# Kernel tuning notes

Measured on AMD Instinct MI355X. Metric: run time of the kernel, lower is better.

The kernel has to match this reference:

```python
import jax, jax.numpy as jnp
import numpy as np

N = 100000
E = 1600000
IN_DIM, H1, H2, H3 = 128, 128, 64, 32


def gcn_conv(x, edge_index, W, b, n):
    # PyG GCNConv (default): add self-loops, symmetric norm D^-1/2 (A+I) D^-1/2,
    # out[dst] = sum_{src->dst} norm * (x @ W)[src] + b
    src, dst = edge_index[0], edge_index[1]
    loops = jnp.arange(n)
    src = jnp.concatenate([src, loops])
    dst = jnp.concatenate([dst, loops])
    deg = jax.ops.segment_sum(jnp.ones((src.shape[0],), dtype=x.dtype), dst, num_segments=n)
    dinv = jnp.where(deg > 0, jax.lax.rsqrt(deg), jnp.zeros((), dtype=x.dtype))
    norm = dinv[src] * dinv[dst]  # [E+N]
    h = x @ W                      # [N, out_dim] dense transform first (out_dim <= in_dim)
    msg = h[src] * norm[:, None]   # [E+N, out_dim] gather + scale
    out = jax.ops.segment_sum(msg, dst, num_segments=n)
    return out + b


def setup_inputs() -> dict:
    key = jax.random.key(0)
    ks = jax.random.split(key, 10)
    def glorot(k, shape):
        lim = np.sqrt(6.0 / (shape[0] + shape[1]))
        return jax.random.uniform(k, shape, jnp.float32, -lim, lim)
    return {
        "x": jax.random.normal(ks[0], (N, IN_DIM), jnp.float32),
        "edge_index": jax.random.randint(ks[1], (2, E), 0, N, jnp.int64),
        "W1": glorot(ks[2], (IN_DIM, H1)), "b1": jnp.zeros((H1,), jnp.float32),
        "W2": glorot(ks[3], (H1, H2)),     "b2": jnp.zeros((H2,), jnp.float32),
        "W3": glorot(ks[4], (H2, H3)),     "b3": jnp.zeros((H3,), jnp.float32),
        "Wl": glorot(ks[5], (H3, 1)),      "bl": jnp.zeros((1,), jnp.float32),
    }


def reference(x, edge_index, W1, b1, W2, b2, W3, b3, Wl, bl):
    n = x.shape[0]
    h = jax.nn.relu(gcn_conv(x, edge_index, W1, b1, n))   # dropout p=0.5 is identity in eval
    h = jax.nn.relu(gcn_conv(h, edge_index, W2, b2, n))
    h = jax.nn.relu(gcn_conv(h, edge_index, W3, b3, n))
    return jax.nn.sigmoid(h @ Wl + bl)                    # [N, 1]
```

## Files before the change

kernel.cpp:

```cpp
#include <hip/hip_runtime.h>
#include <hip/hip_fp16.h>
#include <math.h>


#define BSHIFT 8
#define BNODES (1 << BSHIFT)
#define SRCBITS 17
#define MAXB 512

union H8 { float4 f4; __half2 h2[4]; };

typedef _Float16 half8 __attribute__((ext_vector_type(8)));
typedef float floatx4 __attribute__((ext_vector_type(4)));


__global__ __launch_bounds__(256) void k_hist(const int* __restrict__ dst, int E,
                                              int* __restrict__ bucketcnt, int B) {
    __shared__ int h[MAXB];
    int tid = threadIdx.x;
    h[tid] = 0; h[tid + 256] = 0;
    __syncthreads();
    for (int i = blockIdx.x * 256 + tid; i < E; i += gridDim.x * 256)
        atomicAdd(&h[dst[i] >> BSHIFT], 1);
    __syncthreads();
    if (tid < B && h[tid] > 0) atomicAdd(&bucketcnt[tid], h[tid]);
    int t2 = tid + 256;
    if (t2 < B && h[t2] > 0) atomicAdd(&bucketcnt[t2], h[t2]);
}

__global__ __launch_bounds__(512) void k_bscan(const int* __restrict__ bucketcnt,
                                               int* __restrict__ bucketbase,
                                               int* __restrict__ bucketfill,
                                               int* __restrict__ row_ptr,
                                               int B, int n, int E) {
    __shared__ int s[MAXB];
    int tid = threadIdx.x;
    int v = (tid < B) ? bucketcnt[tid] : 0;
    s[tid] = v;
    __syncthreads();
    for (int off = 1; off < MAXB; off <<= 1) {
        int t = (tid >= off) ? s[tid - off] : 0;
        __syncthreads();
        s[tid] += t;
        __syncthreads();
    }
    int excl = s[tid] - v;
    if (tid < B) { bucketbase[tid] = excl; bucketfill[tid] = excl; }
    if (tid == 0) { bucketbase[B] = E; row_ptr[n] = E; }
}

__global__ __launch_bounds__(256) void k_bucket(const int* __restrict__ src,
                                                const int* __restrict__ dst, int E,
                                                int* __restrict__ bucketfill,
                                                unsigned int* __restrict__ edgebuf,
                                                int B) {
    __shared__ int h[MAXB];
    __shared__ int cursor[MAXB];
    int tid = threadIdx.x;
    int base = blockIdx.x * 4096;
    int end = min(base + 4096, E);
    h[tid] = 0; h[tid + 256] = 0;
    __syncthreads();
    for (int i = base + tid; i < end; i += 256)
        atomicAdd(&h[dst[i] >> BSHIFT], 1);
    __syncthreads();
    if (tid < B) cursor[tid] = (h[tid] > 0) ? atomicAdd(&bucketfill[tid], h[tid]) : 0;
    int t2 = tid + 256;
    if (t2 < B) cursor[t2] = (h[t2] > 0) ? atomicAdd(&bucketfill[t2], h[t2]) : 0;
    __syncthreads();
    for (int i = base + tid; i < end; i += 256) {
        int d = dst[i];
        int b = d >> BSHIFT;
        unsigned int pk = ((unsigned int)(d & (BNODES - 1)) << SRCBITS) | (unsigned int)src[i];
        int pos = atomicAdd(&cursor[b], 1);
        edgebuf[pos] = pk;
    }
}

__global__ __launch_bounds__(256) void k_build(const unsigned int* __restrict__ edgebuf,
                                               const int* __restrict__ bucketbase,
                                               int* __restrict__ row_ptr,
                                               float* __restrict__ dinv,
                                               int* __restrict__ col, int n) {
    __shared__ int cnt[BNODES];
    __shared__ int s[BNODES];
    int b = blockIdx.x;
    int tid = threadIdx.x;
    int node0 = b << BSHIFT;
    int ebase = bucketbase[b], eend = bucketbase[b + 1];
    cnt[tid] = 0;
    __syncthreads();
    for (int i = ebase + tid; i < eend; i += 256)
        atomicAdd(&cnt[edgebuf[i] >> SRCBITS], 1);
    __syncthreads();
    int c = cnt[tid];
    s[tid] = c;
    __syncthreads();
    for (int off = 1; off < 256; off <<= 1) {
        int t = (tid >= off) ? s[tid - off] : 0;
        __syncthreads();
        s[tid] += t;
        __syncthreads();
    }
    int p = ebase + s[tid] - c;
    int node = node0 + tid;
    if (node < n) { row_ptr[node] = p; dinv[node] = rsqrtf((float)(c + 1)); }
    cnt[tid] = p;
    __syncthreads();
    for (int i = ebase + tid; i < eend; i += 256) {
        unsigned int pk = edgebuf[i];
        int pos = atomicAdd(&cnt[pk >> SRCBITS], 1);
        col[pos] = (int)(pk & ((1u << SRCBITS) - 1));
    }
}

__global__ void k_packW3(const float* __restrict__ W1, const float* __restrict__ W2,
                         const float* __restrict__ W3, _Float16* __restrict__ P1,
                         _Float16* __restrict__ P2, _Float16* __restrict__ P3) {
    int e = blockIdx.x * 256 + threadIdx.x;
    const float* W; _Float16* P; int OUT, idx;
    if (e < 16384)      { W = W1; P = P1; OUT = 128; idx = e; }
    else if (e < 24576) { W = W2; P = P2; OUT = 64;  idx = e - 16384; }
    else if (e < 26624) { W = W3; P = P3; OUT = 32;  idx = e - 24576; }
    else return;
    int j = idx & 7;
    int lane = (idx >> 3) & 63;
    int rest = idx >> 9;
    int NT = OUT >> 4;
    int t = rest % NT;
    int ss = rest / NT;
    int k = ss * 32 + (lane >> 4) * 8 + j;
    int nn = t * 16 + (lane & 15);
    P[idx] = (_Float16)W[k * OUT + nn];
}

template <int IN, int OUT>
__global__ __launch_bounds__(256) void k_matmul_mfma(const float* __restrict__ x,
                                                     const _Float16* __restrict__ Wpk,
                                                     const float* __restrict__ dinv,
                                                     __half* __restrict__ out, int n) {
    constexpr int S = IN / 32;
    constexpr int NT = OUT / 16;
    constexpr int LDH = IN + 8;
    __shared__ _Float16 xs[64 * LDH];

    int tid = threadIdx.x;
    int rowbase = blockIdx.x * 64;

    constexpr int TOT = 64 * IN / 8;
    const float4* x4 = (const float4*)x;
    for (int i = tid; i < TOT; i += 256) {
        int r = i / (IN / 8), kg = i % (IN / 8);
        int row = rowbase + r;
        float4 a = make_float4(0.f, 0.f, 0.f, 0.f), b = a;
        if (row < n) {
            a = x4[(size_t)row * (IN / 4) + kg * 2 + 0];
            b = x4[(size_t)row * (IN / 4) + kg * 2 + 1];
        }
        _Float16* p = &xs[r * LDH + kg * 8];
        p[0] = (_Float16)a.x; p[1] = (_Float16)a.y;
        p[2] = (_Float16)a.z; p[3] = (_Float16)a.w;
        p[4] = (_Float16)b.x; p[5] = (_Float16)b.y;
        p[6] = (_Float16)b.z; p[7] = (_Float16)b.w;
    }
    __syncthreads();

    int lane = tid & 63;
    int wave = tid >> 6;
    int m = lane & 15, quad = lane >> 4;

    floatx4 acc[NT];
#pragma unroll
    for (int t = 0; t < NT; ++t) acc[t] = (floatx4){0.f, 0.f, 0.f, 0.f};

    const half8* Wf = (const half8*)Wpk;
#pragma unroll
    for (int s = 0; s < S; ++s) {
        half8 a = *(const half8*)&xs[(wave * 16 + m) * LDH + s * 32 + quad * 8];
#pragma unroll
        for (int t = 0; t < NT; ++t) {
            half8 b = Wf[(s * NT + t) * 64 + lane];
            acc[t] = __builtin_amdgcn_mfma_f32_16x16x32_f16(a, b, acc[t], 0, 0, 0);
        }
    }

    int rbase = rowbase + wave * 16 + quad * 4;
#pragma unroll
    for (int r = 0; r < 4; ++r) {
        int row = rbase + r;
        if (row < n) {
            float dsc = dinv[row];
#pragma unroll
            for (int t = 0; t < NT; ++t)
                out[(size_t)row * OUT + t * 16 + m] = __float2half(acc[t][r] * dsc);
        }
    }
}

template <int F, int OUT>
__global__ __launch_bounds__(256) void k_agg_mm(const __half* __restrict__ hs,
                                                const float* __restrict__ dinv,
                                                const float* __restrict__ bias,
                                                const int* __restrict__ row_ptr,
                                                const int* __restrict__ col,
                                                const _Float16* __restrict__ Wpk,
                                                __half* __restrict__ out, int n) {
    constexpr int S = F / 32;
    constexpr int NT = OUT / 16;
    constexpr int LDH = F + 8;
    constexpr int LPN = F / 8;
    __shared__ _Float16 zs[64 * LDH];

    int tid = threadIdx.x;
    int rowbase = blockIdx.x * 64;
    const float4* h4 = (const float4*)hs;

    for (int task = tid; task < 64 * LPN; task += 256) {
        int nl = task / LPN;
        int fg = task % LPN;
        int node = rowbase + nl;
        H8 o;
        if (node < n) {
            float acc[8];
            H8 u;
            u.f4 = h4[(size_t)node * LPN + fg];
#pragma unroll
            for (int q = 0; q < 4; ++q) {
                float2 f = __half22float2(u.h2[q]);
                acc[2 * q + 0] = f.x;
                acc[2 * q + 1] = f.y;
            }
            int beg = row_ptr[node], end = row_ptr[node + 1];
            int j = beg;
            for (; j + 3 < end; j += 4) {
                int s0 = col[j], s1 = col[j + 1], s2 = col[j + 2], s3 = col[j + 3];
                H8 u0, u1, u2, u3;
                u0.f4 = h4[(size_t)s0 * LPN + fg];
                u1.f4 = h4[(size_t)s1 * LPN + fg];
                u2.f4 = h4[(size_t)s2 * LPN + fg];
                u3.f4 = h4[(size_t)s3 * LPN + fg];
#pragma unroll
                for (int q = 0; q < 4; ++q) {
                    float2 f0 = __half22float2(u0.h2[q]);
                    float2 f1 = __half22float2(u1.h2[q]);
                    float2 f2 = __half22float2(u2.h2[q]);
                    float2 f3 = __half22float2(u3.h2[q]);
                    acc[2 * q + 0] += (f0.x + f1.x) + (f2.x + f3.x);
                    acc[2 * q + 1] += (f0.y + f1.y) + (f2.y + f3.y);
                }
            }
            for (; j < end; ++j) {
                H8 u2;
                u2.f4 = h4[(size_t)col[j] * LPN + fg];
#pragma unroll
                for (int q = 0; q < 4; ++q) {
                    float2 f = __half22float2(u2.h2[q]);
                    acc[2 * q + 0] += f.x;
                    acc[2 * q + 1] += f.y;
                }
            }
            float dsc = dinv[node];
#pragma unroll
            for (int q = 0; q < 4; ++q) {
                float v0 = fmaxf(fmaf(acc[2 * q + 0], dsc, bias[fg * 8 + 2 * q + 0]), 0.f);
                float v1 = fmaxf(fmaf(acc[2 * q + 1], dsc, bias[fg * 8 + 2 * q + 1]), 0.f);
                o.h2[q] = __floats2half2_rn(v0, v1);
            }
        } else {
            o.f4 = make_float4(0.f, 0.f, 0.f, 0.f);
        }
        *(float4*)&zs[nl * LDH + fg * 8] = o.f4;
    }
    __syncthreads();

    int lane = tid & 63;
    int wave = tid >> 6;
    int m = lane & 15, quad = lane >> 4;

    floatx4 acc[NT];
#pragma unroll
    for (int t = 0; t < NT; ++t) acc[t] = (floatx4){0.f, 0.f, 0.f, 0.f};

    const half8* Wf = (const half8*)Wpk;
#pragma unroll
    for (int s = 0; s < S; ++s) {
        half8 a = *(const half8*)&zs[(wave * 16 + m) * LDH + s * 32 + quad * 8];
#pragma unroll
        for (int t = 0; t < NT; ++t) {
            half8 b = Wf[(s * NT + t) * 64 + lane];
            acc[t] = __builtin_amdgcn_mfma_f32_16x16x32_f16(a, b, acc[t], 0, 0, 0);
        }
    }

    int rbase = rowbase + wave * 16 + quad * 4;
#pragma unroll
    for (int r = 0; r < 4; ++r) {
        int row = rbase + r;
        if (row < n) {
            float dsc = dinv[row];
#pragma unroll
            for (int t = 0; t < NT; ++t)
                out[(size_t)row * OUT + t * 16 + m] = __float2half(acc[t][r] * dsc);
        }
    }
}

__global__ __launch_bounds__(256) void k_agg_final(const __half* __restrict__ hs,
                                                   const float* __restrict__ dinv,
                                                   const float* __restrict__ bias,
                                                   const int* __restrict__ row_ptr,
                                                   const int* __restrict__ col,
                                                   const float* __restrict__ Wl,
                                                   const float* __restrict__ bl,
                                                   float* __restrict__ out, int n) {
    constexpr int LPN = 4;
    int t = blockIdx.x * 256 + threadIdx.x;
    int node = t / LPN;
    int fg = t % LPN;
    if (node >= n) return;

    const float4* h4 = (const float4*)hs;
    float acc[8];
    {
        H8 u;
        u.f4 = h4[(size_t)node * LPN + fg];
#pragma unroll
        for (int q = 0; q < 4; ++q) {
            float2 f = __half22float2(u.h2[q]);
            acc[2 * q + 0] = f.x;
            acc[2 * q + 1] = f.y;
        }
    }
    int beg = row_ptr[node], end = row_ptr[node + 1];
    int j = beg;
    for (; j + 3 < end; j += 4) {
        int s0 = col[j], s1 = col[j + 1], s2 = col[j + 2], s3 = col[j + 3];
        H8 u0, u1, u2, u3;
        u0.f4 = h4[(size_t)s0 * LPN + fg];
        u1.f4 = h4[(size_t)s1 * LPN + fg];
        u2.f4 = h4[(size_t)s2 * LPN + fg];
        u3.f4 = h4[(size_t)s3 * LPN + fg];
#pragma unroll
        for (int q = 0; q < 4; ++q) {
            float2 f0 = __half22float2(u0.h2[q]);
            float2 f1 = __half22float2(u1.h2[q]);
            float2 f2 = __half22float2(u2.h2[q]);
            float2 f3 = __half22float2(u3.h2[q]);
            acc[2 * q + 0] += (f0.x + f1.x) + (f2.x + f3.x);
            acc[2 * q + 1] += (f0.y + f1.y) + (f2.y + f3.y);
        }
    }
    for (; j < end; ++j) {
        H8 u;
        u.f4 = h4[(size_t)col[j] * LPN + fg];
#pragma unroll
        for (int q = 0; q < 4; ++q) {
            float2 f = __half22float2(u.h2[q]);
            acc[2 * q + 0] += f.x;
            acc[2 * q + 1] += f.y;
        }
    }
    float dsc = dinv[node];
    float partial = 0.f;
#pragma unroll
    for (int k = 0; k < 8; ++k) {
        float v = fmaxf(fmaf(acc[k], dsc, bias[fg * 8 + k]), 0.f);
        partial = fmaf(v, Wl[fg * 8 + k], partial);
    }
    partial += __shfl_xor(partial, 1);
    partial += __shfl_xor(partial, 2);
    if (fg == 0) out[node] = 1.f / (1.f + expf(-(partial + bl[0])));
}

extern "C" void kernel_launch(void* const* d_in, const int* in_sizes, int n_in,
                              void* d_out, int out_size, void* d_ws, size_t ws_size,
                              hipStream_t stream) {
    const float* x  = (const float*)d_in[0];
    const int*   ei = (const int*)d_in[1];
    const float* W1 = (const float*)d_in[2];
    const float* b1 = (const float*)d_in[3];
    const float* W2 = (const float*)d_in[4];
    const float* b2 = (const float*)d_in[5];
    const float* W3 = (const float*)d_in[6];
    const float* b3 = (const float*)d_in[7];
    const float* Wl = (const float*)d_in[8];
    const float* bl = (const float*)d_in[9];

    const int N = in_sizes[0] / 128;
    const int E = in_sizes[1] / 2;
    const int* src = ei;
    const int* dst = ei + E;
    const int B = (N + BNODES - 1) >> BSHIFT;

    char* ws = (char*)d_ws;
    size_t off = 0;
    auto take = [&](size_t bytes) -> char* {
        char* p = ws + off;
        off += (bytes + 255) & ~(size_t)255;
        return p;
    };
    int*          bucketcnt  = (int*)take(MAXB * 4);
    int*          bucketbase = (int*)take((MAXB + 1) * 4);
    int*          bucketfill = (int*)take(MAXB * 4);
    unsigned int* edgebuf    = (unsigned int*)take((size_t)E * 4);
    int*          row_ptr    = (int*)take((size_t)(N + 1) * 4);
    float*        dinv       = (float*)take((size_t)N * 4);
    int*          col        = (int*)take((size_t)E * 4);
    __half*       bufA       = (__half*)take((size_t)N * 128 * 2);
    __half*       bufB       = (__half*)take((size_t)N * 128 * 2);
    _Float16*     Wpk1       = (_Float16*)take(128 * 128 * 2);
    _Float16*     Wpk2       = (_Float16*)take(128 * 64 * 2);
    _Float16*     Wpk3       = (_Float16*)take(64 * 32 * 2);
    (void)ws_size;

    hipMemsetAsync(bucketcnt, 0, MAXB * 4, stream);

    int gM = (N + 63) / 64;

    k_hist<<<512, 256, 0, stream>>>(dst, E, bucketcnt, B);
    k_bscan<<<1, MAXB, 0, stream>>>(bucketcnt, bucketbase, bucketfill, row_ptr, B, N, E);
    k_bucket<<<(E + 4095) / 4096, 256, 0, stream>>>(src, dst, E, bucketfill, edgebuf, B);
    k_build<<<B, 256, 0, stream>>>(edgebuf, bucketbase, row_ptr, dinv, col, N);

    k_packW3<<<(26624 + 255) / 256, 256, 0, stream>>>(W1, W2, W3, Wpk1, Wpk2, Wpk3);

    k_matmul_mfma<128, 128><<<gM, 256, 0, stream>>>(x, Wpk1, dinv, bufA, N);

    k_agg_mm<128, 64><<<gM, 256, 0, stream>>>(bufA, dinv, b1, row_ptr, col, Wpk2, bufB, N);

    k_agg_mm<64, 32><<<gM, 256, 0, stream>>>(bufB, dinv, b2, row_ptr, col, Wpk3, bufA, N);

    k_agg_final<<<((size_t)N * 4 + 255) / 256, 256, 0, stream>>>(
        bufA, dinv, b3, row_ptr, col, Wl, bl, (float*)d_out, N);
}
```

Baseline: 291.2 us.

## Halve row tile per block and split output tiles across wave pairs

Reduces the per-block row tile from 64 to 32 in the dense MFMA matmul and the fused aggregate+matmul kernels. Pairs of waves now share a 16-row slab and each computes half of the output column tiles, and the grid doubles. The aim is more blocks and fewer serial gather tasks per thread in the latency-bound aggregation, plus lower LDS and register use for better occupancy. In exchange, weight fragments are reloaded by twice as many blocks and per-block fixed overhead doubles.

```diff
diff --git a/kernel.cpp b/kernel.cpp
--- a/kernel.cpp
+++ b/kernel.cpp
@@ -141,13 +141,14 @@
                                                      __half* __restrict__ out, int n) {
     constexpr int S = IN / 32;
     constexpr int NT = OUT / 16;
+    constexpr int TPW = NT / 2;
     constexpr int LDH = IN + 8;
-    __shared__ _Float16 xs[64 * LDH];
-
-    int tid = threadIdx.x;
-    int rowbase = blockIdx.x * 64;
-
-    constexpr int TOT = 64 * IN / 8;
+    __shared__ _Float16 xs[32 * LDH];
+
+    int tid = threadIdx.x;
+    int rowbase = blockIdx.x * 32;
+
+    constexpr int TOT = 32 * IN / 8;
     const float4* x4 = (const float4*)x;
     for (int i = tid; i < TOT; i += 256) {
         int r = i / (IN / 8), kg = i % (IN / 8);
@@ -168,31 +169,33 @@
     int lane = tid & 63;
     int wave = tid >> 6;
     int m = lane & 15, quad = lane >> 4;
-
-    floatx4 acc[NT];
-#pragma unroll
-    for (int t = 0; t < NT; ++t) acc[t] = (floatx4){0.f, 0.f, 0.f, 0.f};
+    int rg = wave >> 1;
+    int th = wave & 1;
+
+    floatx4 acc[TPW];
+#pragma unroll
+    for (int t = 0; t < TPW; ++t) acc[t] = (floatx4){0.f, 0.f, 0.f, 0.f};
 
     const half8* Wf = (const half8*)Wpk;
 #pragma unroll
     for (int s = 0; s < S; ++s) {
-        half8 a = *(const half8*)&xs[(wave * 16 + m) * LDH + s * 32 + quad * 8];
-#pragma unroll
-        for (int t = 0; t < NT; ++t) {
-            half8 b = Wf[(s * NT + t) * 64 + lane];
+        half8 a = *(const half8*)&xs[(rg * 16 + m) * LDH + s * 32 + quad * 8];
+#pragma unroll
+        for (int t = 0; t < TPW; ++t) {
+            half8 b = Wf[(s * NT + th * TPW + t) * 64 + lane];
             acc[t] = __builtin_amdgcn_mfma_f32_16x16x32_f16(a, b, acc[t], 0, 0, 0);
         }
     }
 
-    int rbase = rowbase + wave * 16 + quad * 4;
+    int rbase = rowbase + rg * 16 + quad * 4;
 #pragma unroll
     for (int r = 0; r < 4; ++r) {
         int row = rbase + r;
         if (row < n) {
             float dsc = dinv[row];
 #pragma unroll
-            for (int t = 0; t < NT; ++t)
-                out[(size_t)row * OUT + t * 16 + m] = __float2half(acc[t][r] * dsc);
+            for (int t = 0; t < TPW; ++t)
+                out[(size_t)row * OUT + (th * TPW + t) * 16 + m] = __float2half(acc[t][r] * dsc);
         }
     }
 }
@@ -207,15 +210,16 @@
                                                 __half* __restrict__ out, int n) {
     constexpr int S = F / 32;
     constexpr int NT = OUT / 16;
+    constexpr int TPW = NT / 2;
     constexpr int LDH = F + 8;
     constexpr int LPN = F / 8;
-    __shared__ _Float16 zs[64 * LDH];
-
-    int tid = threadIdx.x;
-    int rowbase = blockIdx.x * 64;
+    __shared__ _Float16 zs[32 * LDH];
+
+    int tid = threadIdx.x;
+    int rowbase = blockIdx.x * 32;
     const float4* h4 = (const float4*)hs;
 
-    for (int task = tid; task < 64 * LPN; task += 256) {
+    for (int task = tid; task < 32 * LPN; task += 256) {
         int nl = task / LPN;
         int fg = task % LPN;
         int node = rowbase + nl;
@@ -276,31 +280,33 @@
     int lane = tid & 63;
     int wave = tid >> 6;
     int m = lane & 15, quad = lane >> 4;
-
-    floatx4 acc[NT];
-#pragma unroll
-    for (int t = 0; t < NT; ++t) acc[t] = (floatx4){0.f, 0.f, 0.f, 0.f};
+    int rg = wave >> 1;
+    int th = wave & 1;
+
+    floatx4 acc[TPW];
+#pragma unroll
+    for (int t = 0; t < TPW; ++t) acc[t] = (floatx4){0.f, 0.f, 0.f, 0.f};
 
     const half8* Wf = (const half8*)Wpk;
 #pragma unroll
     for (int s = 0; s < S; ++s) {
-        half8 a = *(const half8*)&zs[(wave * 16 + m) * LDH + s * 32 + quad * 8];
-#pragma unroll
-        for (int t = 0; t < NT; ++t) {
-            half8 b = Wf[(s * NT + t) * 64 + lane];
+        half8 a = *(const half8*)&zs[(rg * 16 + m) * LDH + s * 32 + quad * 8];
+#pragma unroll
+        for (int t = 0; t < TPW; ++t) {
+            half8 b = Wf[(s * NT + th * TPW + t) * 64 + lane];
             acc[t] = __builtin_amdgcn_mfma_f32_16x16x32_f16(a, b, acc[t], 0, 0, 0);
         }
     }
 
-    int rbase = rowbase + wave * 16 + quad * 4;
+    int rbase = rowbase + rg * 16 + quad * 4;
 #pragma unroll
     for (int r = 0; r < 4; ++r) {
         int row = rbase + r;
         if (row < n) {
             float dsc = dinv[row];
 #pragma unroll
-            for (int t = 0; t < NT; ++t)
-                out[(size_t)row * OUT + t * 16 + m] = __float2half(acc[t][r] * dsc);
+            for (int t = 0; t < TPW; ++t)
+                out[(size_t)row * OUT + (th * TPW + t) * 16 + m] = __float2half(acc[t][r] * dsc);
         }
     }
 }
@@ -415,7 +421,7 @@
 
     hipMemsetAsync(bucketcnt, 0, MAXB * 4, stream);
 
-    int gM = (N + 63) / 64;
+    int gM = (N + 31) / 32;
 
     k_hist<<<512, 256, 0, stream>>>(dst, E, bucketcnt, B);
     k_bscan<<<1, MAXB, 0, stream>>>(bucketcnt, bucketbase, bucketfill, row_ptr, B, N, E);
```

Result: no change. 288.1 us (-1.1%).
